# Kernel optimization log

Measured on AMD Instinct MI355X. Metric: run time of the kernel, lower is better.

## Reference

```python
import jax, jax.numpy as jnp
import numpy as np

MARGIN = 0.3
PD_EPS = 1e-6  # torch F.pairwise_distance adds eps to the difference


def setup_inputs() -> dict:
    key = jax.random.key(0)
    k1, k2 = jax.random.split(key)
    B, D, NUM_CLASSES = 8192, 256, 8
    embeddings = jax.random.normal(k1, (B, D), dtype=jnp.float32)
    labels = jax.random.randint(k2, (B,), 0, NUM_CLASSES, dtype=jnp.int64)
    return {"embeddings": embeddings, "labels": labels}


def _pairwise_euclidean(x):
    # cdist(x, x, p=2) via the Gram trick; clamp tiny negatives before sqrt
    sq = jnp.sum(x * x, axis=1)  # [B]
    d2 = sq[:, None] + sq[None, :] - 2.0 * (x @ x.T)
    return jnp.sqrt(jnp.maximum(d2, 0.0))


def reference(embeddings, labels):
    B = embeddings.shape[0]
    D = _pairwise_euclidean(embeddings)  # [B, B]

    eq = labels[:, None] == labels[None, :]
    eye = jnp.eye(B, dtype=bool)
    pos_mask = eq & ~eye          # same label, not self
    neg_mask = ~eq                # different label

    # hard mining: per anchor, farthest positive and closest negative
    pos_idx = jnp.argmax(jnp.where(pos_mask, D, -jnp.inf), axis=1)  # [B]
    neg_idx = jnp.argmin(jnp.where(neg_mask, D, jnp.inf), axis=1)   # [B]
    valid = pos_mask.any(axis=1) & neg_mask.any(axis=1)             # [B]

    # recompute triplet distances like F.pairwise_distance (eps on the diff)
    pos_dist = jnp.linalg.norm(embeddings - embeddings[pos_idx] + PD_EPS, axis=1)
    neg_dist = jnp.linalg.norm(embeddings - embeddings[neg_idx] + PD_EPS, axis=1)

    per_anchor = jax.nn.relu(pos_dist - neg_dist + MARGIN)
    n_valid = jnp.maximum(valid.sum(), 1)
    loss = jnp.sum(jnp.where(valid, per_anchor, 0.0)) / n_valid.astype(per_anchor.dtype)
    return loss
```

## Files before the change

kernel.cpp:

```cpp
#include <hip/hip_runtime.h>
#include <math.h>


typedef __attribute__((ext_vector_type(8))) short short8;
typedef __attribute__((ext_vector_type(4))) float floatx4;

#define B_N 8192
#define D_K 256

__device__ __forceinline__ unsigned short f2bf_rne(float f) {
  unsigned u = __float_as_uint(f);
  u += 0x7FFFu + ((u >> 16) & 1u);
  return (unsigned short)(u >> 16);
}

#define DPP_SHR(x, CTRL) \
  ((unsigned)__builtin_amdgcn_update_dpp((int)(x), (int)(x), (CTRL), 0xF, 0xF, false))

__global__ void k_split(const float* __restrict__ x, unsigned short* __restrict__ xhf,
                        float* __restrict__ sqq,
                        float* __restrict__ sum, int* __restrict__ cnt,
                        int* __restrict__ done) {
  __shared__ float sw[64];
  const int tid  = threadIdx.x;
  const int lane = tid & 63;
  const int w    = tid >> 6;
  const int b    = blockIdx.x;
  const int m    = lane & 15;
  const int quad = lane >> 4;
  const int row  = b * 16 + m;

  float s = 0.f;
#pragma unroll
  for (int h = 0; h < 2; ++h) {
    int tk = w + h * 4;
    int kk = tk * 32 + quad * 8;
    float4 f0 = *reinterpret_cast<const float4*>(x + (size_t)row * D_K + kk);
    float4 f1 = *reinterpret_cast<const float4*>(x + (size_t)row * D_K + kk + 4);
    s += f0.x * f0.x + f0.y * f0.y + f0.z * f0.z + f0.w * f0.w;
    s += f1.x * f1.x + f1.y * f1.y + f1.z * f1.z + f1.w * f1.w;
    ushort4 lo, hi;
    lo.x = f2bf_rne(f0.x); lo.y = f2bf_rne(f0.y); lo.z = f2bf_rne(f0.z); lo.w = f2bf_rne(f0.w);
    hi.x = f2bf_rne(f1.x); hi.y = f2bf_rne(f1.y); hi.z = f2bf_rne(f1.z); hi.w = f2bf_rne(f1.w);
    size_t o = ((size_t)b * 8 + tk) * 512 + lane * 8;
    *reinterpret_cast<ushort4*>(xhf + o)     = lo;
    *reinterpret_cast<ushort4*>(xhf + o + 4) = hi;
  }
  s += __shfl_xor(s, 16);
  s += __shfl_xor(s, 32);
  if (quad == 0) sw[w * 16 + m] = s;
  __syncthreads();
  if (tid < 16) {
    int i = b * 16 + tid;
    float t = sw[tid] + sw[16 + tid] + sw[32 + tid] + sw[48 + tid];
    sqq[i] = fmaf(t, 128.f, 262144.f);
  }
  if (b == 0 && tid == 0) { *sum = 0.f; *cnt = 0; *done = 0; }
}

__global__ __launch_bounds__(256, 6) void k_mine16(
    const unsigned short* __restrict__ xhf, const int* __restrict__ lab,
    const float* __restrict__ sqq,
    unsigned* __restrict__ ppart, unsigned* __restrict__ npart) {
  __shared__ unsigned jbp[4 * 64], jbn[4 * 64];

  int t  = blockIdx.x;
  const int hb = t & 1;
  t >>= 1;
  int bi = (int)(64.5f - sqrtf(64.5f * 64.5f - 2.f * (float)t));
  int b0 = 64 * bi - (bi * (bi - 1)) / 2;
  if (t < b0) { bi--; b0 = 64 * bi - (bi * (bi - 1)) / 2; }
  else {
    int b1 = 64 * (bi + 1) - ((bi + 1) * bi) / 2;
    if (t >= b1) { bi++; b0 = b1; }
  }
  const int bj = bi + (t - b0);

  const int tid  = threadIdx.x;
  const int lane = tid & 63;
  const int w    = tid >> 6;
  const int wi   = w >> 1;
  const int wj   = w & 1;
  const int quad = lane >> 4, l15 = lane & 15;
  const int i0   = bi * 128 + hb * 64 + wi * 32;

  unsigned lip = 0;
  float    sqi[8];
#pragma unroll
  for (int r = 0; r < 8; ++r) {
    int ir = i0 + (r >> 2) * 16 + quad * 4 + (r & 3);
    lip |= ((unsigned)lab[ir] & 0xFu) << (r * 4);
    sqi[r] = sqq[ir];
  }

  const unsigned aoff = (unsigned)(i0 >> 4) * 4096u + (unsigned)lane * 8u;
  const unsigned boff = (unsigned)(bj * 8 + wj * 4) * 4096u + (unsigned)lane * 8u;

  floatx4 acc[8];
#pragma unroll
  for (int q = 0; q < 8; ++q) acc[q] = (floatx4)0.f;

#pragma unroll
  for (int tk = 0; tk < 8; ++tk) {
    short8 Bf[4];
#pragma unroll
    for (int nt = 0; nt < 4; ++nt)
      Bf[nt] = *reinterpret_cast<const short8*>(xhf + boff + (unsigned)(nt * 4096 + tk * 512));
    short8 Af[2];
#pragma unroll
    for (int mt = 0; mt < 2; ++mt)
      Af[mt] = *reinterpret_cast<const short8*>(xhf + aoff + (unsigned)(mt * 4096 + tk * 512));
#pragma unroll
    for (int mt = 0; mt < 2; ++mt)
#pragma unroll
      for (int nt = 0; nt < 4; ++nt)
        acc[mt * 4 + nt] = __builtin_amdgcn_mfma_f32_16x16x32_bf16(
            Af[mt], Bf[nt], acc[mt * 4 + nt], 0, 0, 0);
  }

  unsigned pkey[8], nkey[8];
#pragma unroll
  for (int r = 0; r < 8; ++r) { pkey[r] = 0u; nkey[r] = 0xFFFFFFFFu; }

#pragma unroll
  for (int nt = 0; nt < 4; ++nt) {
    int      j  = bj * 128 + wj * 64 + nt * 16 + l15;
    unsigned jl = (unsigned)lab[j] & 0xFu;
    float    sj = sqq[j];
    unsigned jp = 0u, jn = 0xFFFFFFFFu;
#pragma unroll
    for (int r = 0; r < 8; ++r) {
      float dot = acc[(r >> 2) * 4 + nt][r & 3];
      int   ir  = i0 + (r >> 2) * 16 + quad * 4 + (r & 3);
      bool  eq  = (jl == ((lip >> (r * 4)) & 0xFu));
      unsigned kqi  = (unsigned)fmaf(-256.f, dot, sj);
      unsigned keyi = (kqi << 13) | (unsigned)j;
      unsigned pci = eq ? keyi : 0u;
      unsigned nci = eq ? 0xFFFFFFFFu : keyi;
      pkey[r] = pkey[r] > pci ? pkey[r] : pci;
      nkey[r] = nkey[r] < nci ? nkey[r] : nci;
      unsigned kqj  = (unsigned)fmaf(-256.f, dot, sqi[r]);
      unsigned keyj = (kqj << 13) | (unsigned)ir;
      unsigned pcj = eq ? keyj : 0u;
      unsigned ncj = eq ? 0xFFFFFFFFu : keyj;
      jp = jp > pcj ? jp : pcj;
      jn = jn < ncj ? jn : ncj;
    }
#pragma unroll
    for (int m = 16; m < 64; m <<= 1) {
      unsigned op = (unsigned)__shfl_xor((int)jp, m);
      unsigned on = (unsigned)__shfl_xor((int)jn, m);
      jp = jp > op ? jp : op;
      jn = jn < on ? jn : on;
    }
    if (quad == 0) {
      jbp[w * 64 + nt * 16 + l15] = jp;
      jbn[w * 64 + nt * 16 + l15] = jn;
    }
  }

#pragma unroll
  for (int r = 0; r < 8; ++r) {
    unsigned tp = DPP_SHR(pkey[r], 0x118); pkey[r] = pkey[r] > tp ? pkey[r] : tp;
    unsigned tn = DPP_SHR(nkey[r], 0x118); nkey[r] = nkey[r] < tn ? nkey[r] : tn;
  }
#pragma unroll
  for (int r = 0; r < 8; ++r) {
    unsigned tp = DPP_SHR(pkey[r], 0x114); pkey[r] = pkey[r] > tp ? pkey[r] : tp;
    unsigned tn = DPP_SHR(nkey[r], 0x114); nkey[r] = nkey[r] < tn ? nkey[r] : tn;
  }
#pragma unroll
  for (int r = 0; r < 8; ++r) {
    unsigned tp = DPP_SHR(pkey[r], 0x112); pkey[r] = pkey[r] > tp ? pkey[r] : tp;
    unsigned tn = DPP_SHR(nkey[r], 0x112); nkey[r] = nkey[r] < tn ? nkey[r] : tn;
  }
#pragma unroll
  for (int r = 0; r < 8; ++r) {
    unsigned tp = DPP_SHR(pkey[r], 0x111); pkey[r] = pkey[r] > tp ? pkey[r] : tp;
    unsigned tn = DPP_SHR(nkey[r], 0x111); nkey[r] = nkey[r] < tn ? nkey[r] : tn;
  }
#pragma unroll
  for (int r = 0; r < 8; ++r) {
    if (l15 == 15) {
      int ir = i0 + (r >> 2) * 16 + quad * 4 + (r & 3);
      size_t idx = (size_t)(2 * bj + wj) * B_N + ir;
      ppart[idx] = pkey[r];
      npart[idx] = nkey[r];
    }
  }

  __syncthreads();
  if (wi == 0 && bi != bj) {
    unsigned p  = jbp[w * 64 + lane];
    unsigned n  = jbn[w * 64 + lane];
    unsigned p2 = jbp[(w + 2) * 64 + lane];
    unsigned n2 = jbn[(w + 2) * 64 + lane];
    p = p > p2 ? p : p2;
    n = n < n2 ? n : n2;
    int j = bj * 128 + wj * 64 + lane;
    size_t idx = (size_t)(2 * bi + hb) * B_N + j;
    ppart[idx] = p;
    npart[idx] = n;
  }
}

__global__ void k_finish(const float* __restrict__ x,
                         const unsigned* __restrict__ ppart,
                         const unsigned* __restrict__ npart,
                         float* __restrict__ sum, int* __restrict__ cnt,
                         int* __restrict__ done, float* __restrict__ out) {
  __shared__ unsigned spk[32], snk[32];
  __shared__ float ssum[4];
  __shared__ int   scnt[4];
  const int tid = threadIdx.x;
  const int a0  = blockIdx.x * 32;

  if (tid < 32) { spk[tid] = 0u; snk[tid] = 0xFFFFFFFFu; }
  __syncthreads();

  {
    const int a    = a0 + (tid & 31);
    const int part = tid >> 5;
    unsigned p = 0u, n = 0xFFFFFFFFu;
#pragma unroll
    for (int s = 0; s < 16; ++s) {
      size_t idx = (size_t)(part * 16 + s) * B_N + a;
      unsigned pv = ppart[idx];
      unsigned nv = npart[idx];
      p = p > pv ? p : pv;
      n = n < nv ? n : nv;
    }
    atomicMax(&spk[tid & 31], p);
    atomicMin(&snk[tid & 31], n);
  }
  __syncthreads();

  const int w = tid >> 6, lane = tid & 63;
  float lsum = 0.f; int lcnt = 0;
#pragma unroll
  for (int it = 0; it < 8; ++it) {
    int al = w * 8 + it;
    int a  = a0 + al;
    unsigned p = spk[al];
    unsigned n = snk[al];
    bool valid = (p != 0u) && (n != 0xFFFFFFFFu);
    int  pidx = valid ? (int)(p & 8191u) : 0;
    int  nidx = valid ? (int)(n & 8191u) : 0;

    float4 xa = *reinterpret_cast<const float4*>(x + (size_t)a * D_K + lane * 4);
    float4 xp = *reinterpret_cast<const float4*>(x + (size_t)pidx * D_K + lane * 4);
    float4 xn = *reinterpret_cast<const float4*>(x + (size_t)nidx * D_K + lane * 4);
    float dx, sp = 0.f, sn = 0.f;
    dx = xa.x - xp.x + 1e-6f; sp = fmaf(dx, dx, sp);
    dx = xa.y - xp.y + 1e-6f; sp = fmaf(dx, dx, sp);
    dx = xa.z - xp.z + 1e-6f; sp = fmaf(dx, dx, sp);
    dx = xa.w - xp.w + 1e-6f; sp = fmaf(dx, dx, sp);
    dx = xa.x - xn.x + 1e-6f; sn = fmaf(dx, dx, sn);
    dx = xa.y - xn.y + 1e-6f; sn = fmaf(dx, dx, sn);
    dx = xa.z - xn.z + 1e-6f; sn = fmaf(dx, dx, sn);
    dx = xa.w - xn.w + 1e-6f; sn = fmaf(dx, dx, sn);
#pragma unroll
    for (int o = 32; o > 0; o >>= 1) {
      sp += __shfl_down(sp, o, 64);
      sn += __shfl_down(sn, o, 64);
    }
    if (lane == 0 && valid) {
      float per = sqrtf(sp) - sqrtf(sn) + 0.3f;
      if (per > 0.f) lsum += per;
      lcnt += 1;
    }
  }
  if (lane == 0) { ssum[w] = lsum; scnt[w] = lcnt; }
  __syncthreads();
  if (tid == 0) {
    atomicAdd(sum, ssum[0] + ssum[1] + ssum[2] + ssum[3]);
    atomicAdd(cnt, scnt[0] + scnt[1] + scnt[2] + scnt[3]);
    __threadfence();
    int prev = atomicAdd(done, 1);
    if (prev == gridDim.x - 1) {
      float s = atomicAdd(sum, 0.f);
      int   cc = atomicAdd(cnt, 0);
      if (cc < 1) cc = 1;
      out[0] = s / (float)cc;
    }
  }
}

extern "C" void kernel_launch(void* const* d_in, const int* in_sizes, int n_in,
                              void* d_out, int out_size, void* d_ws, size_t ws_size,
                              hipStream_t stream) {
  const float* x   = (const float*)d_in[0];
  const int*   lab = (const int*)d_in[1];
  float*       out = (float*)d_out;

  char* ws = (char*)d_ws;
  unsigned short* xhf = (unsigned short*)ws;
  float* sqq = (float*)(ws + (size_t)4608 * 1024);
  char*  pb = ws + (size_t)4608 * 1024 + 65536;
  size_t seg = (size_t)128 * B_N * 4;
  unsigned* ppart = (unsigned*)(pb);
  unsigned* npart = (unsigned*)(pb + seg);
  float* sum  = (float*)(pb + 2 * seg);
  int*   cnt  = (int*)(sum + 1);
  int*   done = (int*)(sum + 2);

  k_split<<<B_N / 16, 256, 0, stream>>>(x, xhf, sqq, sum, cnt, done);
  k_mine16<<<4160, 256, 0, stream>>>(xhf, lab, sqq, ppart, npart);
  k_finish<<<B_N / 32, 256, 0, stream>>>(x, ppart, npart, sum, cnt, done, out);
}
```

Before: 121.8 us.

## Sort rows by label to specialize mining tiles into pos-only or neg-only

Two small kernels build a counting-sort permutation of rows by label. The permutation is applied when converting embeddings to bf16 and when gathering rows in the finish kernel. Because rows are grouped by class, each 128x128 tile in the mining kernel can check its label range and pick a specialized epilogue. Tiles whose label ranges do not overlap track only the negative min, single-label tiles track only the positive max, and only tiles on class boundaries run the full masked code. This is meant to roughly halve the key/compare/shuffle epilogue work, at the cost of two extra kernel launches and an indirect index lookup in the split and finish kernels.

Result: slower. 124.4 us (+2.1%).

```diff
diff --git a/kernel.cpp b/kernel.cpp
--- a/kernel.cpp
+++ b/kernel.cpp
@@ -17,7 +17,52 @@
 #define DPP_SHR(x, CTRL) \
   ((unsigned)__builtin_amdgcn_update_dpp((int)(x), (int)(x), (CTRL), 0xF, 0xF, false))
 
-__global__ void k_split(const float* __restrict__ x, unsigned short* __restrict__ xhf,
+__global__ void k_hist(const int* __restrict__ lab, int* __restrict__ chunkhist) {
+  __shared__ int h[8];
+  const int tid = threadIdx.x, b = blockIdx.x;
+  if (tid < 8) h[tid] = 0;
+  __syncthreads();
+  atomicAdd(&h[lab[b * 256 + tid] & 7], 1);
+  __syncthreads();
+  if (tid < 8) chunkhist[b * 8 + tid] = h[tid];
+}
+
+__global__ void k_perm(const int* __restrict__ lab, const int* __restrict__ chunkhist,
+                       int* __restrict__ perm, int* __restrict__ labp) {
+  __shared__ int ch[256];
+  __shared__ int base[8];
+  __shared__ int wcnt[4][8];
+  const int tid = threadIdx.x, b = blockIdx.x;
+  ch[tid] = chunkhist[tid];
+  __syncthreads();
+  if (tid < 8) {
+    const int c = tid;
+    int acc = 0;
+    for (int cc = 0; cc < c; ++cc)
+      for (int k = 0; k < 32; ++k) acc += ch[k * 8 + cc];
+    for (int k = 0; k < b; ++k) acc += ch[k * 8 + c];
+    base[c] = acc;
+  }
+  const int i    = b * 256 + tid;
+  const int myc  = lab[i] & 7;
+  const int lane = tid & 63, w = tid >> 6;
+  unsigned long long bal[8];
+#pragma unroll
+  for (int c = 0; c < 8; ++c) bal[c] = __ballot(myc == c);
+  if (lane == 0) {
+#pragma unroll
+    for (int c = 0; c < 8; ++c) wcnt[w][c] = (int)__popcll(bal[c]);
+  }
+  __syncthreads();
+  int rank = (int)__popcll(bal[myc] & ((1ull << lane) - 1ull));
+  for (int ww = 0; ww < w; ++ww) rank += wcnt[ww][myc];
+  const int pos = base[myc] + rank;
+  perm[pos] = i;
+  labp[pos] = myc;
+}
+
+__global__ void k_split(const float* __restrict__ x, const int* __restrict__ perm,
+                        unsigned short* __restrict__ xhf,
                         float* __restrict__ sqq,
                         float* __restrict__ sum, int* __restrict__ cnt,
                         int* __restrict__ done) {
@@ -29,14 +74,15 @@
   const int m    = lane & 15;
   const int quad = lane >> 4;
   const int row  = b * 16 + m;
+  const int rsrc = perm[row];
 
   float s = 0.f;
 #pragma unroll
   for (int h = 0; h < 2; ++h) {
     int tk = w + h * 4;
     int kk = tk * 32 + quad * 8;
-    float4 f0 = *reinterpret_cast<const float4*>(x + (size_t)row * D_K + kk);
-    float4 f1 = *reinterpret_cast<const float4*>(x + (size_t)row * D_K + kk + 4);
+    float4 f0 = *reinterpret_cast<const float4*>(x + (size_t)rsrc * D_K + kk);
+    float4 f1 = *reinterpret_cast<const float4*>(x + (size_t)rsrc * D_K + kk + 4);
     s += f0.x * f0.x + f0.y * f0.y + f0.z * f0.z + f0.w * f0.w;
     s += f1.x * f1.x + f1.y * f1.y + f1.z * f1.z + f1.w * f1.w;
     ushort4 lo, hi;
@@ -58,8 +104,127 @@
   if (b == 0 && tid == 0) { *sum = 0.f; *cnt = 0; *done = 0; }
 }
 
+template <int MODE>
+__device__ __forceinline__ void mine_tail(
+    const floatx4* acc, const int* __restrict__ labp, const float* __restrict__ sqq,
+    const float* sqi, int i0, int bi, int bj, int hb, int w, int lane,
+    unsigned* jbp, unsigned* jbn,
+    unsigned* __restrict__ ppart, unsigned* __restrict__ npart) {
+  const int wi = w >> 1, wj = w & 1;
+  const int quad = lane >> 4, l15 = lane & 15;
+
+  unsigned lip = 0;
+  if (MODE == 2) {
+#pragma unroll
+    for (int r = 0; r < 8; ++r) {
+      int ir = i0 + (r >> 2) * 16 + quad * 4 + (r & 3);
+      lip |= ((unsigned)labp[ir] & 0xFu) << (r * 4);
+    }
+  }
+
+  unsigned pkey[8], nkey[8];
+#pragma unroll
+  for (int r = 0; r < 8; ++r) { pkey[r] = 0u; nkey[r] = 0xFFFFFFFFu; }
+
+#pragma unroll
+  for (int nt = 0; nt < 4; ++nt) {
+    int      j  = bj * 128 + wj * 64 + nt * 16 + l15;
+    float    sj = sqq[j];
+    unsigned jl = (MODE == 2) ? ((unsigned)labp[j] & 0xFu) : 0u;
+    unsigned jp = 0u, jn = 0xFFFFFFFFu;
+#pragma unroll
+    for (int r = 0; r < 8; ++r) {
+      float dot = acc[(r >> 2) * 4 + nt][r & 3];
+      int   ir  = i0 + (r >> 2) * 16 + quad * 4 + (r & 3);
+      unsigned keyi = ((unsigned)fmaf(-256.f, dot, sj) << 13) | (unsigned)j;
+      unsigned keyj = ((unsigned)fmaf(-256.f, dot, sqi[r]) << 13) | (unsigned)ir;
+      if (MODE == 2) {
+        bool eq = (jl == ((lip >> (r * 4)) & 0xFu));
+        unsigned pci = eq ? keyi : 0u;
+        unsigned nci = eq ? 0xFFFFFFFFu : keyi;
+        pkey[r] = pkey[r] > pci ? pkey[r] : pci;
+        nkey[r] = nkey[r] < nci ? nkey[r] : nci;
+        unsigned pcj = eq ? keyj : 0u;
+        unsigned ncj = eq ? 0xFFFFFFFFu : keyj;
+        jp = jp > pcj ? jp : pcj;
+        jn = jn < ncj ? jn : ncj;
+      } else if (MODE == 1) {
+        pkey[r] = pkey[r] > keyi ? pkey[r] : keyi;
+        jp = jp > keyj ? jp : keyj;
+      } else {
+        nkey[r] = nkey[r] < keyi ? nkey[r] : keyi;
+        jn = jn < keyj ? jn : keyj;
+      }
+    }
+#pragma unroll
+    for (int m = 16; m < 64; m <<= 1) {
+      if (MODE != 0) {
+        unsigned op = (unsigned)__shfl_xor((int)jp, m);
+        jp = jp > op ? jp : op;
+      }
+      if (MODE != 1) {
+        unsigned on = (unsigned)__shfl_xor((int)jn, m);
+        jn = jn < on ? jn : on;
+      }
+    }
+    if (quad == 0) {
+      if (MODE != 0) jbp[w * 64 + nt * 16 + l15] = jp;
+      if (MODE != 1) jbn[w * 64 + nt * 16 + l15] = jn;
+    }
+  }
+
+#pragma unroll
+  for (int r = 0; r < 8; ++r) {
+    if (MODE != 0) { unsigned tp = DPP_SHR(pkey[r], 0x118); pkey[r] = pkey[r] > tp ? pkey[r] : tp; }
+    if (MODE != 1) { unsigned tn = DPP_SHR(nkey[r], 0x118); nkey[r] = nkey[r] < tn ? nkey[r] : tn; }
+  }
+#pragma unroll
+  for (int r = 0; r < 8; ++r) {
+    if (MODE != 0) { unsigned tp = DPP_SHR(pkey[r], 0x114); pkey[r] = pkey[r] > tp ? pkey[r] : tp; }
+    if (MODE != 1) { unsigned tn = DPP_SHR(nkey[r], 0x114); nkey[r] = nkey[r] < tn ? nkey[r] : tn; }
+  }
+#pragma unroll
+  for (int r = 0; r < 8; ++r) {
+    if (MODE != 0) { unsigned tp = DPP_SHR(pkey[r], 0x112); pkey[r] = pkey[r] > tp ? pkey[r] : tp; }
+    if (MODE != 1) { unsigned tn = DPP_SHR(nkey[r], 0x112); nkey[r] = nkey[r] < tn ? nkey[r] : tn; }
+  }
+#pragma unroll
+  for (int r = 0; r < 8; ++r) {
+    if (MODE != 0) { unsigned tp = DPP_SHR(pkey[r], 0x111); pkey[r] = pkey[r] > tp ? pkey[r] : tp; }
+    if (MODE != 1) { unsigned tn = DPP_SHR(nkey[r], 0x111); nkey[r] = nkey[r] < tn ? nkey[r] : tn; }
+  }
+#pragma unroll
+  for (int r = 0; r < 8; ++r) {
+    if (l15 == 15) {
+      int ir = i0 + (r >> 2) * 16 + quad * 4 + (r & 3);
+      size_t idx = (size_t)(2 * bj + wj) * B_N + ir;
+      ppart[idx] = (MODE == 0) ? 0u : pkey[r];
+      npart[idx] = (MODE == 1) ? 0xFFFFFFFFu : nkey[r];
+    }
+  }
+
+  __syncthreads();
+  if (wi == 0 && bi != bj) {
+    unsigned p = 0u, n = 0xFFFFFFFFu;
+    if (MODE != 0) {
+      p = jbp[w * 64 + lane];
+      unsigned p2 = jbp[(w + 2) * 64 + lane];
+      p = p > p2 ? p : p2;
+    }
+    if (MODE != 1) {
+      n = jbn[w * 64 + lane];
+      unsigned n2 = jbn[(w + 2) * 64 + lane];
+      n = n < n2 ? n : n2;
+    }
+    int j = bj * 128 + wj * 64 + lane;
+    size_t idx = (size_t)(2 * bi + hb) * B_N + j;
+    ppart[idx] = p;
+    npart[idx] = n;
+  }
+}
+
 __global__ __launch_bounds__(256, 6) void k_mine16(
-    const unsigned short* __restrict__ xhf, const int* __restrict__ lab,
+    const unsigned short* __restrict__ xhf, const int* __restrict__ labp,
     const float* __restrict__ sqq,
     unsigned* __restrict__ ppart, unsigned* __restrict__ npart) {
   __shared__ unsigned jbp[4 * 64], jbn[4 * 64];
@@ -81,17 +246,18 @@
   const int w    = tid >> 6;
   const int wi   = w >> 1;
   const int wj   = w & 1;
-  const int quad = lane >> 4, l15 = lane & 15;
+  const int quad = lane >> 4;
   const int i0   = bi * 128 + hb * 64 + wi * 32;
 
-  unsigned lip = 0;
-  float    sqi[8];
-#pragma unroll
-  for (int r = 0; r < 8; ++r) {
-    int ir = i0 + (r >> 2) * 16 + quad * 4 + (r & 3);
-    lip |= ((unsigned)lab[ir] & 0xFu) << (r * 4);
-    sqi[r] = sqq[ir];
-  }
+  float sqi[8];
+#pragma unroll
+  for (int r = 0; r < 8; ++r)
+    sqi[r] = sqq[i0 + (r >> 2) * 16 + quad * 4 + (r & 3)];
+
+  const int la0 = labp[bi * 128 + hb * 64];
+  const int la1 = labp[bi * 128 + hb * 64 + 63];
+  const int lb0 = labp[bj * 128];
+  const int lb1 = labp[bj * 128 + 127];
 
   const unsigned aoff = (unsigned)(i0 >> 4) * 4096u + (unsigned)lane * 8u;
   const unsigned boff = (unsigned)(bj * 8 + wj * 4) * 4096u + (unsigned)lane * 8u;
@@ -109,7 +275,7 @@
     short8 Af[2];
 #pragma unroll
     for (int mt = 0; mt < 2; ++mt)
-      Af[mt] = *reinterpret_cast<const short8*>(xhf + aoff + (unsigned)(mt * 4096 + tk * 512));
+      Af[mt] = *reinterpret_cast<const short8*>(xhf + aoff + (unsigned)(mt * 8 + tk) * 512u);
 #pragma unroll
     for (int mt = 0; mt < 2; ++mt)
 #pragma unroll
@@ -118,93 +284,16 @@
             Af[mt], Bf[nt], acc[mt * 4 + nt], 0, 0, 0);
   }
 
-  unsigned pkey[8], nkey[8];
-#pragma unroll
-  for (int r = 0; r < 8; ++r) { pkey[r] = 0u; nkey[r] = 0xFFFFFFFFu; }
-
-#pragma unroll
-  for (int nt = 0; nt < 4; ++nt) {
-    int      j  = bj * 128 + wj * 64 + nt * 16 + l15;
-    unsigned jl = (unsigned)lab[j] & 0xFu;
-    float    sj = sqq[j];
-    unsigned jp = 0u, jn = 0xFFFFFFFFu;
-#pragma unroll
-    for (int r = 0; r < 8; ++r) {
-      float dot = acc[(r >> 2) * 4 + nt][r & 3];
-      int   ir  = i0 + (r >> 2) * 16 + quad * 4 + (r & 3);
-      bool  eq  = (jl == ((lip >> (r * 4)) & 0xFu));
-      unsigned kqi  = (unsigned)fmaf(-256.f, dot, sj);
-      unsigned keyi = (kqi << 13) | (unsigned)j;
-      unsigned pci = eq ? keyi : 0u;
-      unsigned nci = eq ? 0xFFFFFFFFu : keyi;
-      pkey[r] = pkey[r] > pci ? pkey[r] : pci;
-      nkey[r] = nkey[r] < nci ? nkey[r] : nci;
-      unsigned kqj  = (unsigned)fmaf(-256.f, dot, sqi[r]);
-      unsigned keyj = (kqj << 13) | (unsigned)ir;
-      unsigned pcj = eq ? keyj : 0u;
-      unsigned ncj = eq ? 0xFFFFFFFFu : keyj;
-      jp = jp > pcj ? jp : pcj;
-      jn = jn < ncj ? jn : ncj;
-    }
-#pragma unroll
-    for (int m = 16; m < 64; m <<= 1) {
-      unsigned op = (unsigned)__shfl_xor((int)jp, m);
-      unsigned on = (unsigned)__shfl_xor((int)jn, m);
-      jp = jp > op ? jp : op;
-      jn = jn < on ? jn : on;
-    }
-    if (quad == 0) {
-      jbp[w * 64 + nt * 16 + l15] = jp;
-      jbn[w * 64 + nt * 16 + l15] = jn;
-    }
-  }
-
-#pragma unroll
-  for (int r = 0; r < 8; ++r) {
-    unsigned tp = DPP_SHR(pkey[r], 0x118); pkey[r] = pkey[r] > tp ? pkey[r] : tp;
-    unsigned tn = DPP_SHR(nkey[r], 0x118); nkey[r] = nkey[r] < tn ? nkey[r] : tn;
-  }
-#pragma unroll
-  for (int r = 0; r < 8; ++r) {
-    unsigned tp = DPP_SHR(pkey[r], 0x114); pkey[r] = pkey[r] > tp ? pkey[r] : tp;
-    unsigned tn = DPP_SHR(nkey[r], 0x114); nkey[r] = nkey[r] < tn ? nkey[r] : tn;
-  }
-#pragma unroll
-  for (int r = 0; r < 8; ++r) {
-    unsigned tp = DPP_SHR(pkey[r], 0x112); pkey[r] = pkey[r] > tp ? pkey[r] : tp;
-    unsigned tn = DPP_SHR(nkey[r], 0x112); nkey[r] = nkey[r] < tn ? nkey[r] : tn;
-  }
-#pragma unroll
-  for (int r = 0; r < 8; ++r) {
-    unsigned tp = DPP_SHR(pkey[r], 0x111); pkey[r] = pkey[r] > tp ? pkey[r] : tp;
-    unsigned tn = DPP_SHR(nkey[r], 0x111); nkey[r] = nkey[r] < tn ? nkey[r] : tn;
-  }
-#pragma unroll
-  for (int r = 0; r < 8; ++r) {
-    if (l15 == 15) {
-      int ir = i0 + (r >> 2) * 16 + quad * 4 + (r & 3);
-      size_t idx = (size_t)(2 * bj + wj) * B_N + ir;
-      ppart[idx] = pkey[r];
-      npart[idx] = nkey[r];
-    }
-  }
-
-  __syncthreads();
-  if (wi == 0 && bi != bj) {
-    unsigned p  = jbp[w * 64 + lane];
-    unsigned n  = jbn[w * 64 + lane];
-    unsigned p2 = jbp[(w + 2) * 64 + lane];
-    unsigned n2 = jbn[(w + 2) * 64 + lane];
-    p = p > p2 ? p : p2;
-    n = n < n2 ? n : n2;
-    int j = bj * 128 + wj * 64 + lane;
-    size_t idx = (size_t)(2 * bi + hb) * B_N + j;
-    ppart[idx] = p;
-    npart[idx] = n;
-  }
-}
-
-__global__ void k_finish(const float* __restrict__ x,
+  if (la1 < lb0 || lb1 < la0) {
+    mine_tail<0>(acc, labp, sqq, sqi, i0, bi, bj, hb, w, lane, jbp, jbn, ppart, npart);
+  } else if (la0 == lb1 && la1 == lb0) {
+    mine_tail<1>(acc, labp, sqq, sqi, i0, bi, bj, hb, w, lane, jbp, jbn, ppart, npart);
+  } else {
+    mine_tail<2>(acc, labp, sqq, sqi, i0, bi, bj, hb, w, lane, jbp, jbn, ppart, npart);
+  }
+}
+
+__global__ void k_finish(const float* __restrict__ x, const int* __restrict__ perm,
                          const unsigned* __restrict__ ppart,
                          const unsigned* __restrict__ npart,
                          float* __restrict__ sum, int* __restrict__ cnt,
@@ -246,10 +335,11 @@
     bool valid = (p != 0u) && (n != 0xFFFFFFFFu);
     int  pidx = valid ? (int)(p & 8191u) : 0;
     int  nidx = valid ? (int)(n & 8191u) : 0;
-
-    float4 xa = *reinterpret_cast<const float4*>(x + (size_t)a * D_K + lane * 4);
-    float4 xp = *reinterpret_cast<const float4*>(x + (size_t)pidx * D_K + lane * 4);
-    float4 xn = *reinterpret_cast<const float4*>(x + (size_t)nidx * D_K + lane * 4);
+    int  ra = perm[a], rp = perm[pidx], rn = perm[nidx];
+
+    float4 xa = *reinterpret_cast<const float4*>(x + (size_t)ra * D_K + lane * 4);
+    float4 xp = *reinterpret_cast<const float4*>(x + (size_t)rp * D_K + lane * 4);
+    float4 xn = *reinterpret_cast<const float4*>(x + (size_t)rn * D_K + lane * 4);
     float dx, sp = 0.f, sn = 0.f;
     dx = xa.x - xp.x + 1e-6f; sp = fmaf(dx, dx, sp);
     dx = xa.y - xp.y + 1e-6f; sp = fmaf(dx, dx, sp);
@@ -295,6 +385,9 @@
 
   char* ws = (char*)d_ws;
   unsigned short* xhf = (unsigned short*)ws;
+  int* perm      = (int*)(ws + (size_t)4096 * 1024);
+  int* labp      = (int*)(ws + (size_t)4096 * 1024 + 32768);
+  int* chunkhist = (int*)(ws + (size_t)4096 * 1024 + 65536);
   float* sqq = (float*)(ws + (size_t)4608 * 1024);
   char*  pb = ws + (size_t)4608 * 1024 + 65536;
   size_t seg = (size_t)128 * B_N * 4;
@@ -304,7 +397,9 @@
   int*   cnt  = (int*)(sum + 1);
   int*   done = (int*)(sum + 2);
 
-  k_split<<<B_N / 16, 256, 0, stream>>>(x, xhf, sqq, sum, cnt, done);
-  k_mine16<<<4160, 256, 0, stream>>>(xhf, lab, sqq, ppart, npart);
-  k_finish<<<B_N / 32, 256, 0, stream>>>(x, ppart, npart, sum, cnt, done, out);
-}
+  k_hist<<<32, 256, 0, stream>>>(lab, chunkhist);
+  k_perm<<<32, 256, 0, stream>>>(lab, chunkhist, perm, labp);
+  k_split<<<B_N / 16, 256, 0, stream>>>(x, perm, xhf, sqq, sum, cnt, done);
+  k_mine16<<<4160, 256, 0, stream>>>(xhf, labp, sqq, ppart, npart);
+  k_finish<<<B_N / 32, 256, 0, stream>>>(x, perm, ppart, npart, sum, cnt, done, out);
+}
```
